# Optimization experiments

Measured on AMD Instinct MI355X. Metric: run time of the kernel, lower is better.

## Reference

```python
import jax, jax.numpy as jnp
import numpy as np

DIM = 1024
HDS = 16
HEAD_DIM = DIM // HDS
ISC = True


def setup_inputs() -> dict:
    key = jax.random.key(0)
    k = jax.random.split(key, 5)
    x = jax.random.normal(k[0], (4, 2048, DIM), dtype=jnp.float32)
    # Linear(dim, 3*dim): weight [3*dim, dim] (torch layout), bias [3*dim]
    scale = 1.0 / np.sqrt(DIM)
    w_qkv = jax.random.uniform(k[1], (3 * DIM, DIM), jnp.float32, -scale, scale)
    b_qkv = jax.random.uniform(k[2], (3 * DIM,), jnp.float32, -scale, scale)
    w_out = jax.random.uniform(k[3], (DIM, DIM), jnp.float32, -scale, scale)
    b_out = jax.random.uniform(k[4], (DIM,), jnp.float32, -scale, scale)
    return {"x": x, "w_qkv": w_qkv, "b_qkv": b_qkv, "w_out": w_out, "b_out": b_out}


def reference(x, w_qkv, b_qkv, w_out, b_out):
    b, s, dim = x.shape
    # QKV projection: x @ w_qkv.T + b_qkv -> split into q, k, v
    qkv = jnp.einsum('bsd,ed->bse', x, w_qkv) + b_qkv
    q, k, v = jnp.split(qkv, 3, axis=-1)
    # [b, s, dim] -> [b, h, s, hd]
    def to_heads(t):
        return t.reshape(b, s, HDS, HEAD_DIM).transpose(0, 2, 1, 3)
    q, k, v = to_heads(q), to_heads(k), to_heads(v)
    att = jnp.einsum('bhqd,bhkd->bhqk', q, k) * (HEAD_DIM ** -0.5)
    if ISC:
        mask = jnp.triu(jnp.ones((s, s), dtype=bool), k=1)  # True above diagonal
        att = jnp.where(mask[None, None], -jnp.inf, att)
    att = jax.nn.softmax(att, axis=-1)
    # dropout is identity in eval mode
    out = jnp.einsum('bhqk,bhkd->bhqd', att, v)
    out = out.transpose(0, 2, 1, 3).reshape(b, s, dim)
    out = jnp.einsum('bsd,ed->bse', out, w_out) + b_out
    return out
```

## Files before the change

### kernel.cpp

```cpp
#include <hip/hip_runtime.h>
#include <stdint.h>

typedef __bf16 bf16x8 __attribute__((ext_vector_type(8)));
typedef short s16x8 __attribute__((ext_vector_type(8)));
typedef short s16x4 __attribute__((ext_vector_type(4)));
typedef float f32x4 __attribute__((ext_vector_type(4)));
typedef float f32x16 __attribute__((ext_vector_type(16)));
typedef unsigned short u16;

#define K_DIM 1024

static __device__ __forceinline__ u16 f2bf(float f) {
    uint32_t x = __float_as_uint(f);
    x += 0x7fffu + ((x >> 16) & 1u);
    return (u16)(x >> 16);
}

static __device__ __forceinline__ f32x4 mfma16(s16x8 a, s16x8 b, f32x4 c) {
    return __builtin_amdgcn_mfma_f32_16x16x32_bf16(
        __builtin_bit_cast(bf16x8, a), __builtin_bit_cast(bf16x8, b), c, 0, 0, 0);
}

static __device__ __forceinline__ f32x16 mfma32(s16x8 a, s16x8 b, f32x16 c) {
    return __builtin_amdgcn_mfma_f32_32x32x16_bf16(
        __builtin_bit_cast(bf16x8, a), __builtin_bit_cast(bf16x8, b), c, 0, 0, 0);
}

static __device__ __forceinline__ void gload16(const u16* g, u16* l) {
    __builtin_amdgcn_global_load_lds(
        (const __attribute__((address_space(1))) void*)g,
        (__attribute__((address_space(3))) void*)l,
        16, 0, 0);
}

static __device__ __forceinline__ uint32_t cvt_pk_bf16(float lo, float hi) {
    uint32_t r;
    asm("v_cvt_pk_bf16_f32 %0, %1, %2" : "=v"(r) : "v"(lo), "v"(hi));
    return r;
}

static __device__ __forceinline__ void pswap(uint32_t& a, uint32_t& b) {
    asm volatile("v_permlane32_swap_b32 %0, %1" : "+v"(a), "+v"(b));
}

static __device__ __forceinline__ float fexp2(float x) {
#if __has_builtin(__builtin_amdgcn_exp2f)
    return __builtin_amdgcn_exp2f(x);
#else
    return __expf(x * 0.69314718056f);
#endif
}

__global__ void cvt_all(const float* __restrict__ x, const float* __restrict__ wq,
                        const float* __restrict__ wo,
                        u16* __restrict__ xb, u16* __restrict__ wqb,
                        u16* __restrict__ wob) {
    const int stride = gridDim.x * blockDim.x;
    const int tid = blockIdx.x * blockDim.x + threadIdx.x;
    for (int i = tid; i < 2097152; i += stride) {
        float4 f = ((const float4*)x)[i];
        ushort4 o;
        o.x = f2bf(f.x); o.y = f2bf(f.y); o.z = f2bf(f.z); o.w = f2bf(f.w);
        ((ushort4*)xb)[i] = o;
    }
    for (int i = tid; i < 786432; i += stride) {
        float4 f = ((const float4*)wq)[i];
        ushort4 o;
        o.x = f2bf(f.x); o.y = f2bf(f.y); o.z = f2bf(f.z); o.w = f2bf(f.w);
        ((ushort4*)wqb)[i] = o;
    }
    for (int i = tid; i < 262144; i += stride) {
        float4 f = ((const float4*)wo)[i];
        ushort4 o;
        o.x = f2bf(f.x); o.y = f2bf(f.y); o.z = f2bf(f.z); o.w = f2bf(f.w);
        ((ushort4*)wob)[i] = o;
    }
}

__global__ __launch_bounds__(256) void gemm_qkv(
    const u16* __restrict__ A, const u16* __restrict__ B,
    const float* __restrict__ bias,
    u16* __restrict__ qo, u16* __restrict__ ko, u16* __restrict__ vto)
{
    __shared__ u16 smem[32768];
    u16* ct = smem;
    const int tid = threadIdx.x;
    const int w = tid >> 6, l = tid & 63;
    const int lr = l & 15, lc = l >> 4;

    const int f = blockIdx.y * 64 + blockIdx.x;
    const int c = f & 7, j = f >> 3;
    const int m0 = (c * 8 + (j & 7)) * 128;
    const int n0 = (j >> 3) * 128;
    const int wm = (w >> 1) * 64, wn = (w & 1) * 64;

    const int srow = w * 8 + (l >> 3);
    const int scol = ((l & 7) ^ (l >> 3)) * 8;
    const u16* gA = A + (size_t)(m0 + srow) * K_DIM + scol;
    const u16* gB = B + (size_t)(n0 + srow) * K_DIM + scol;

    f32x4 acc[4][4] = {};

    auto stage = [&](int k0, int buf) {
        u16* base = smem + buf * 16384;
        #pragma unroll
        for (int g = 0; g < 4; ++g) {
            gload16(gA + (size_t)g * 32 * K_DIM + k0, base + (g * 32 + w * 8) * 64);
            gload16(gB + (size_t)g * 32 * K_DIM + k0, base + 8192 + (g * 32 + w * 8) * 64);
        }
    };

    stage(0, 0);
    int cur = 0;

    for (int k0 = 0; k0 < K_DIM; k0 += 64) {
        __syncthreads();
        if (k0 + 64 < K_DIM) stage(k0 + 64, cur ^ 1);
        const u16* As = smem + cur * 16384;
        const u16* Bs = As + 8192;
        #pragma unroll
        for (int kk = 0; kk < 2; ++kk) {
            s16x8 a[4], b[4];
            #pragma unroll
            for (int i = 0; i < 4; ++i) {
                const int row = wm + i * 16 + lr;
                a[i] = *(const s16x8*)&As[row * 64 + ((kk * 32 + lc * 8) ^ ((row & 7) * 8))];
            }
            #pragma unroll
            for (int jn = 0; jn < 4; ++jn) {
                const int row = wn + jn * 16 + lr;
                b[jn] = *(const s16x8*)&Bs[row * 64 + ((kk * 32 + lc * 8) ^ ((row & 7) * 8))];
            }
            #pragma unroll
            for (int i = 0; i < 4; ++i)
                #pragma unroll
                for (int jn = 0; jn < 4; ++jn)
                    acc[i][jn] = mfma16(a[i], b[jn], acc[i][jn]);
        }
        cur ^= 1;
    }

    const int sec = n0 >> 10;
    const int bb = m0 >> 11, s0 = m0 & 2047;

    if (sec < 2) {
        #pragma unroll
        for (int jn = 0; jn < 4; ++jn) {
            const int n = n0 + wn + jn * 16 + lr;
            const float bv = bias[n];
            const int h = (n & 1023) >> 6, d = n & 63;
            #pragma unroll
            for (int i = 0; i < 4; ++i) {
                #pragma unroll
                for (int r = 0; r < 4; ++r) {
                    const int m = m0 + wm + i * 16 + lc * 4 + r;
                    const int s = m & 2047;
                    float v = acc[i][jn][r] + bv;
                    if (sec == 0)
                        qo[((size_t)((bb * 16 + h) * 2048 + s)) * 64 + d] = f2bf(v * 0.18033688f);
                    else
                        ko[((size_t)((bb * 16 + h) * 2048 + s)) * 64 + d] = f2bf(v);
                }
            }
        }
    } else {
        __syncthreads();
        #pragma unroll
        for (int jj = 0; jj < 4; ++jj) {
            const int nl = (wn >> 6) * 16 + lr;
            const float bv = bias[n0 + wn + jj * 16 + lr];
            #pragma unroll
            for (int i = 0; i < 4; ++i) {
                const int mloc = wm + i * 16 + lc * 4;
                uint2 pk;
                pk.x = cvt_pk_bf16(acc[i][jj][0] + bv, acc[i][jj][1] + bv);
                pk.y = cvt_pk_bf16(acc[i][jj][2] + bv, acc[i][jj][3] + bv);
                *(s16x4*)&ct[nl * 136 + mloc] = __builtin_bit_cast(s16x4, pk);
            }
            __syncthreads();
            #pragma unroll
            for (int rep = 0; rep < 2; ++rep) {
                const int col = tid >> 3;
                const int seg = (tid & 7) + rep * 8;
                const int nn = n0 + (col >> 4) * 64 + jj * 16 + (col & 15);
                const int h = (nn & 1023) >> 6, d = nn & 63;
                const int mo = seg * 8;
                s16x8 v = *(const s16x8*)&ct[col * 136 + mo];
                *(s16x8*)&vto[((size_t)((bb * 16 + h) * 64 + d)) * 2048 + s0 + mo] = v;
            }
            __syncthreads();
        }
    }
}

__global__ __launch_bounds__(256, 2) void attn_fwd(
    const u16* __restrict__ q, const u16* __restrict__ k,
    const u16* __restrict__ vt, u16* __restrict__ ao)
{
    __shared__ u16 kt[2][8 * 512];
    __shared__ u16 vtl[2][8 * 512];
    const int w = threadIdx.x >> 6, l = threadIdx.x & 63;
    const int l31 = l & 31, hl = l >> 5;
    const int bh = blockIdx.x;
    const int cp = blockIdx.y;
    const u16* qp = q + (size_t)bh * 2048 * 64;
    const u16* kp = k + (size_t)bh * 2048 * 64;
    const u16* vp = vt + (size_t)bh * 64 * 2048;
    const int bb = bh >> 4, hd = bh & 15;

    for (int pass = 0; pass < 2; ++pass) {
        const int C = pass ? (15 - cp) : cp;
        const int q0 = C * 128 + w * 32;
        const int nb = 2 * C + 2;
        const int diag = 2 * C + (w >> 1);

        s16x8 aQ[4];
        #pragma unroll
        for (int kk = 0; kk < 4; ++kk)
            aQ[kk] = *(const s16x8*)&qp[(q0 + l31) * 64 + kk * 16 + hl * 8];

        f32x16 O[2] = {};
        f32x16 ls16 = {};

        auto stage = [&](int t, int buf) {
            const int c0 = t * 64;
            if (w < 2) {
                #pragma unroll
                for (int gi = 0; gi < 4; ++gi) {
                    const int g = w * 4 + gi;
                    const int jx = g >> 2, kk = g & 3;
                    gload16(kp + (c0 + jx * 32 + l31) * 64 + kk * 16 + hl * 8,
                            &kt[buf][g * 512]);
                }
            } else {
                #pragma unroll
                for (int gi = 0; gi < 4; ++gi) {
                    const int g = (w - 2) * 4 + gi;
                    const int jd = g >> 2, ks = g & 3;
                    gload16(vp + (jd * 32 + l31) * 2048 + c0 + ks * 16 + hl * 8,
                            &vtl[buf][g * 512]);
                }
            }
        };

        __syncthreads();
        stage(0, 0);
        int cur = 0;

        for (int t = 0; t < nb; ++t) {
            __syncthreads();
            if (t + 1 < nb) stage(t + 1, cur ^ 1);

            if (t <= diag) {
                const int c0 = t * 64;
                f32x16 s[2] = {};
                __builtin_amdgcn_s_setprio(1);
                #pragma unroll
                for (int jx = 0; jx < 2; ++jx)
                    #pragma unroll
                    for (int kk = 0; kk < 4; ++kk) {
                        s16x8 kf = *(const s16x8*)&kt[cur][(jx * 4 + kk) * 512 + l * 8];
                        s[jx] = mfma32(kf, aQ[kk], s[jx]);
                    }
                __builtin_amdgcn_s_setprio(0);
                if (t == diag) {
                    const int qrow = q0 + l31;
                    #pragma unroll
                    for (int jx = 0; jx < 2; ++jx)
                        #pragma unroll
                        for (int reg = 0; reg < 16; ++reg) {
                            const int kv = c0 + jx * 32 + (reg & 3) + 8 * (reg >> 2) + 4 * hl;
                            if (kv > qrow) s[jx][reg] = -1e30f;
                        }
                }
                #pragma unroll
                for (int jx = 0; jx < 2; ++jx)
                    #pragma unroll
                    for (int reg = 0; reg < 16; ++reg)
                        s[jx][reg] = fexp2(s[jx][reg]);
                ls16 += s[0] + s[1];
                s16x8 ap[4];
                #pragma unroll
                for (int ks = 0; ks < 4; ++ks) {
                    const int jxs = ks >> 1, b8 = (ks & 1) * 8;
                    uint32_t XA = cvt_pk_bf16(s[jxs][b8 + 0], s[jxs][b8 + 1]);
                    uint32_t XB = cvt_pk_bf16(s[jxs][b8 + 2], s[jxs][b8 + 3]);
                    uint32_t YA = cvt_pk_bf16(s[jxs][b8 + 4], s[jxs][b8 + 5]);
                    uint32_t YB = cvt_pk_bf16(s[jxs][b8 + 6], s[jxs][b8 + 7]);
                    pswap(XA, YA);
                    pswap(XB, YB);
                    uint4 wds = make_uint4(XA, XB, YA, YB);
                    ap[ks] = __builtin_bit_cast(s16x8, wds);
                }
                __builtin_amdgcn_s_setprio(1);
                #pragma unroll
                for (int jd = 0; jd < 2; ++jd)
                    #pragma unroll
                    for (int ks = 0; ks < 4; ++ks) {
                        s16x8 vf = *(const s16x8*)&vtl[cur][(jd * 4 + ks) * 512 + l * 8];
                        O[jd] = mfma32(ap[ks], vf, O[jd]);
                    }
                __builtin_amdgcn_s_setprio(0);
            }
            cur ^= 1;
        }

        float t2 = 0.f;
        #pragma unroll
        for (int e = 0; e < 16; ++e) t2 += ls16[e];
        t2 += __shfl_xor(t2, 32);
        const float lsr = 1.0f / t2;

        float invr[16];
        #pragma unroll
        for (int reg = 0; reg < 16; ++reg)
            invr[reg] = __shfl(lsr, (reg & 3) + 8 * (reg >> 2) + 4 * hl);

        #pragma unroll
        for (int jd = 0; jd < 2; ++jd)
            #pragma unroll
            for (int reg = 0; reg < 16; ++reg) {
                const int qr = (reg & 3) + 8 * (reg >> 2) + 4 * hl;
                ao[((size_t)(bb * 2048 + q0 + qr)) * 1024 + hd * 64 + jd * 32 + l31] =
                    f2bf(O[jd][reg] * invr[reg]);
            }
    }
}

__global__ __launch_bounds__(256) void gemm_out(
    const u16* __restrict__ A, const u16* __restrict__ B,
    const float* __restrict__ bias, float* __restrict__ out)
{
    __shared__ u16 smem[32768];
    const int tid = threadIdx.x;
    const int w = tid >> 6, l = tid & 63;
    const int lr = l & 15, lc = l >> 4;

    const int f = blockIdx.y * 64 + blockIdx.x;
    const int c = f & 7, j = f >> 3;
    const int m0 = (c * 8 + (j & 7)) * 128;
    const int n0 = (j >> 3) * 128;
    const int wm = (w >> 1) * 64, wn = (w & 1) * 64;

    const int srow = w * 8 + (l >> 3);
    const int scol = ((l & 7) ^ (l >> 3)) * 8;
    const u16* gA = A + (size_t)(m0 + srow) * K_DIM + scol;
    const u16* gB = B + (size_t)(n0 + srow) * K_DIM + scol;

    f32x4 acc[4][4] = {};

    auto stage = [&](int k0, int buf) {
        u16* base = smem + buf * 16384;
        #pragma unroll
        for (int g = 0; g < 4; ++g) {
            gload16(gA + (size_t)g * 32 * K_DIM + k0, base + (g * 32 + w * 8) * 64);
            gload16(gB + (size_t)g * 32 * K_DIM + k0, base + 8192 + (g * 32 + w * 8) * 64);
        }
    };

    stage(0, 0);
    int cur = 0;

    for (int k0 = 0; k0 < K_DIM; k0 += 64) {
        __syncthreads();
        if (k0 + 64 < K_DIM) stage(k0 + 64, cur ^ 1);
        const u16* As = smem + cur * 16384;
        const u16* Bs = As + 8192;
        #pragma unroll
        for (int kk = 0; kk < 2; ++kk) {
            s16x8 a[4], b[4];
            #pragma unroll
            for (int i = 0; i < 4; ++i) {
                const int row = wm + i * 16 + lr;
                a[i] = *(const s16x8*)&As[row * 64 + ((kk * 32 + lc * 8) ^ ((row & 7) * 8))];
            }
            #pragma unroll
            for (int jn = 0; jn < 4; ++jn) {
                const int row = wn + jn * 16 + lr;
                b[jn] = *(const s16x8*)&Bs[row * 64 + ((kk * 32 + lc * 8) ^ ((row & 7) * 8))];
            }
            #pragma unroll
            for (int i = 0; i < 4; ++i)
                #pragma unroll
                for (int jn = 0; jn < 4; ++jn)
                    acc[i][jn] = mfma16(a[i], b[jn], acc[i][jn]);
        }
        cur ^= 1;
    }

    #pragma unroll
    for (int jn = 0; jn < 4; ++jn) {
        const int n = n0 + wn + jn * 16 + lr;
        const float bv = bias[n];
        #pragma unroll
        for (int i = 0; i < 4; ++i) {
            #pragma unroll
            for (int r = 0; r < 4; ++r) {
                const int m = m0 + wm + i * 16 + lc * 4 + r;
                out[(size_t)m * 1024 + n] = acc[i][jn][r] + bv;
            }
        }
    }
}

extern "C" void kernel_launch(void* const* d_in, const int* in_sizes, int n_in,
                              void* d_out, int out_size, void* d_ws, size_t ws_size,
                              hipStream_t stream) {
    const float* x     = (const float*)d_in[0];
    const float* w_qkv = (const float*)d_in[1];
    const float* b_qkv = (const float*)d_in[2];
    const float* w_out = (const float*)d_in[3];
    const float* b_out = (const float*)d_in[4];
    float* out = (float*)d_out;

    char* ws = (char*)d_ws;
    u16* xb   = (u16*)(ws);
    u16* wqb  = (u16*)(ws + 16777216);
    u16* wob  = (u16*)(ws + 23068672);
    u16* qws  = (u16*)(ws + 25165824);
    u16* kws  = (u16*)(ws + 41943040);
    u16* vtws = (u16*)(ws + 58720256);
    u16* attn = (u16*)(ws + 75497472);

    cvt_all<<<dim3(2048), 256, 0, stream>>>(x, w_qkv, w_out, xb, wqb, wob);

    gemm_qkv<<<dim3(64, 24), 256, 0, stream>>>(xb, wqb, b_qkv, qws, kws, vtws);
    attn_fwd<<<dim3(64, 8), 256, 0, stream>>>(qws, kws, vtws, attn);
    gemm_out<<<dim3(64, 8), 256, 0, stream>>>(attn, wob, b_out, out);
}
```

Baseline: 133.0 us.

## Triple-buffer K/V tiles in attention with vmcnt-based waits and single barrier

Measured after the change: 133.3 us. About the same (+0.2%).

```diff
diff --git a/kernel.cpp b/kernel.cpp
--- a/kernel.cpp
+++ b/kernel.cpp
@@ -197,8 +197,8 @@
     const u16* __restrict__ q, const u16* __restrict__ k,
     const u16* __restrict__ vt, u16* __restrict__ ao)
 {
-    __shared__ u16 kt[2][8 * 512];
-    __shared__ u16 vtl[2][8 * 512];
+    __shared__ u16 kA[4096], kB[4096], kC[4096];
+    __shared__ u16 vA[4096], vB[4096], vC[4096];
     const int w = threadIdx.x >> 6, l = threadIdx.x & 63;
     const int l31 = l & 31, hl = l >> 5;
     const int bh = blockIdx.x;
@@ -222,7 +222,7 @@
         f32x16 O[2] = {};
         f32x16 ls16 = {};
 
-        auto stage = [&](int t, int buf) {
+        auto stage = [&](int t, u16* kbuf, u16* vbuf) {
             const int c0 = t * 64;
             if (w < 2) {
                 #pragma unroll
@@ -230,7 +230,7 @@
                     const int g = w * 4 + gi;
                     const int jx = g >> 2, kk = g & 3;
                     gload16(kp + (c0 + jx * 32 + l31) * 64 + kk * 16 + hl * 8,
-                            &kt[buf][g * 512]);
+                            &kbuf[g * 512]);
                 }
             } else {
                 #pragma unroll
@@ -238,18 +238,16 @@
                     const int g = (w - 2) * 4 + gi;
                     const int jd = g >> 2, ks = g & 3;
                     gload16(vp + (jd * 32 + l31) * 2048 + c0 + ks * 16 + hl * 8,
-                            &vtl[buf][g * 512]);
+                            &vbuf[g * 512]);
                 }
             }
         };
 
-        __syncthreads();
-        stage(0, 0);
-        int cur = 0;
-
-        for (int t = 0; t < nb; ++t) {
-            __syncthreads();
-            if (t + 1 < nb) stage(t + 1, cur ^ 1);
+        auto iter = [&](int t, const u16* kb, const u16* vb, u16* kn, u16* vn) {
+            if (t + 1 < nb) asm volatile("s_waitcnt vmcnt(4)" ::: "memory");
+            else            asm volatile("s_waitcnt vmcnt(0)" ::: "memory");
+            __builtin_amdgcn_s_barrier();
+            if (t + 2 < nb) stage(t + 2, kn, vn);
 
             if (t <= diag) {
                 const int c0 = t * 64;
@@ -259,7 +257,7 @@
                 for (int jx = 0; jx < 2; ++jx)
                     #pragma unroll
                     for (int kk = 0; kk < 4; ++kk) {
-                        s16x8 kf = *(const s16x8*)&kt[cur][(jx * 4 + kk) * 512 + l * 8];
+                        s16x8 kf = *(const s16x8*)&kb[(jx * 4 + kk) * 512 + l * 8];
                         s[jx] = mfma32(kf, aQ[kk], s[jx]);
                     }
                 __builtin_amdgcn_s_setprio(0);
@@ -297,12 +295,22 @@
                 for (int jd = 0; jd < 2; ++jd)
                     #pragma unroll
                     for (int ks = 0; ks < 4; ++ks) {
-                        s16x8 vf = *(const s16x8*)&vtl[cur][(jd * 4 + ks) * 512 + l * 8];
+                        s16x8 vf = *(const s16x8*)&vb[(jd * 4 + ks) * 512 + l * 8];
                         O[jd] = mfma32(ap[ks], vf, O[jd]);
                     }
                 __builtin_amdgcn_s_setprio(0);
             }
-            cur ^= 1;
+        };
+
+        __syncthreads();
+        stage(0, kA, vA);
+        stage(1, kB, vB);
+
+        int t = 0;
+        while (t < nb) {
+            iter(t, kA, vA, kC, vC); ++t; if (t >= nb) break;
+            iter(t, kB, vB, kA, vA); ++t; if (t >= nb) break;
+            iter(t, kC, vC, kB, vB); ++t;
         }
 
         float t2 = 0.f;
```
